# Kernel optimization log

Hardware: AMD Instinct MI355X
Metric: run time of the kernel (lower is better)

## Reference

```python
import jax, jax.numpy as jnp
import numpy as np

N = 50000      # nodes
E = 800000     # edges (before self-loops)
B = 512        # graphs in batch
IN, HID, OUT, HEADS = 768, 256, 128, 4
NEG_SLOPE = 0.2
EPS = 1e-16


def glorot(key, shape):
    fan = shape[0] + shape[-1]
    return jax.random.normal(key, shape, jnp.float32) * jnp.sqrt(2.0 / fan)


def setup_inputs() -> dict:
    key = jax.random.key(0)
    ks = jax.random.split(key, 12)
    d1, d2 = HID // HEADS, OUT // HEADS
    return {
        "x": jax.random.normal(ks[0], (N, IN), jnp.float32),
        "edge_index": jax.random.randint(ks[1], (2, E), 0, N),
        "batch": jnp.sort(jax.random.randint(ks[2], (N,), 0, B)),
        # conv1: GATConv(IN, HID//HEADS, heads=HEADS)
        "W1": glorot(ks[3], (IN, HID)),
        "att_src1": glorot(ks[4], (HEADS, d1)),
        "att_dst1": glorot(ks[5], (HEADS, d1)),
        "b1": jnp.zeros((HID,), jnp.float32),
        # conv2: GATConv(HID+IN, OUT//HEADS, heads=HEADS)
        "W2": glorot(ks[6], (HID + IN, OUT)),
        "att_src2": glorot(ks[7], (HEADS, d2)),
        "att_dst2": glorot(ks[8], (HEADS, d2)),
        "b2": jnp.zeros((OUT,), jnp.float32),
    }


def gat_conv(x, src, dst, W, att_src, att_dst, bias):
    # PyG GATConv (concat heads): h = x @ W, e_ij = LeakyReLU(a_s.h_j + a_d.h_i),
    # alpha = softmax over incoming edges of each destination node.
    n = x.shape[0]
    heads, d = att_src.shape
    h = (x @ W).reshape(n, heads, d)                          # [N,H,D]
    a_s = jnp.einsum('nhd,hd->nh', h, att_src)                # [N,H]
    a_d = jnp.einsum('nhd,hd->nh', h, att_dst)
    e = jax.nn.leaky_relu(a_s[src] + a_d[dst], NEG_SLOPE)     # [Etot,H]
    e_max = jax.ops.segment_max(e, dst, num_segments=n)
    e = jnp.exp(e - e_max[dst])
    denom = jax.ops.segment_sum(e, dst, num_segments=n)
    alpha = e / (denom[dst] + EPS)                            # [Etot,H]
    msg = h[src] * alpha[:, :, None]                          # [Etot,H,D]
    out = jax.ops.segment_sum(msg, dst, num_segments=n)       # [N,H,D]
    return out.reshape(n, heads * d) + bias


def reference(x, edge_index, batch, W1, att_src1, att_dst1, b1,
              W2, att_src2, att_dst2, b2):
    # BUrumorGAT swaps edge direction: row<->col
    src = edge_index[1]
    dst = edge_index[0]
    # PyG GATConv adds self-loops by default
    loops = jnp.arange(N)
    src = jnp.concatenate([src, loops])
    dst = jnp.concatenate([dst, loops])

    x1 = x  # original features
    h1 = gat_conv(x, src, dst, W1, att_src1, att_dst1, b1)    # [N,HID]
    x2 = h1

    # root of each graph = first node (in order) with that batch id
    roots = jax.ops.segment_min(jnp.arange(N), batch, num_segments=B)  # [B]
    re1 = x1[roots[batch]]                                    # [N,IN]
    xc = jax.nn.relu(jnp.concatenate([h1, re1], axis=1))      # [N,HID+IN]
    # F.dropout with training=False is identity (eval mode)

    h2 = jax.nn.relu(gat_conv(xc, src, dst, W2, att_src2, att_dst2, b2))  # [N,OUT]
    re2 = x2[roots[batch]]                                    # [N,HID]
    feat = jnp.concatenate([h2, re2], axis=1)                 # [N,OUT+HID]

    counts = jax.ops.segment_sum(jnp.ones((N,), jnp.float32), batch, num_segments=B)
    pooled = jax.ops.segment_sum(feat, batch, num_segments=B)
    return pooled / jnp.clip(counts, 1.0)[:, None]            # [B,OUT+HID]
```

## Files before the change

kernel.cpp:

```cpp
#include <hip/hip_runtime.h>

#define NN 50000
#define NBGRAPH 512
#define DIN 768
#define DHID 256
#define DOUT 128

typedef unsigned short ushort_t;
typedef __attribute__((ext_vector_type(4))) float f32x4;
typedef _Float16 f16_t;
typedef __attribute__((ext_vector_type(8))) _Float16 f16x8;

__device__ __forceinline__ float lrelu(float v) { return v > 0.f ? v : 0.2f * v; }

__device__ __forceinline__ float h2f_u(ushort_t u) { return (float)__builtin_bit_cast(f16_t, u); }
__device__ __forceinline__ ushort_t f2h_u(float f) { return __builtin_bit_cast(ushort_t, (f16_t)f); }

__device__ __forceinline__ float sel_h(int h, float q0, float q1, float q2, float q3) {
  float lo = (h & 1) ? q1 : q0;
  float hi = (h & 1) ? q3 : q2;
  return (h & 2) ? hi : lo;
}

__device__ __forceinline__ f16x8 cvt8(float4 u, float4 v) {
  unsigned int a = __builtin_bit_cast(unsigned int, __builtin_amdgcn_cvt_pkrtz(u.x, u.y));
  unsigned int b = __builtin_bit_cast(unsigned int, __builtin_amdgcn_cvt_pkrtz(u.z, u.w));
  unsigned int c = __builtin_bit_cast(unsigned int, __builtin_amdgcn_cvt_pkrtz(v.x, v.y));
  unsigned int d = __builtin_bit_cast(unsigned int, __builtin_amdgcn_cvt_pkrtz(v.z, v.w));
  uint4 q = {a, b, c, d};
  return __builtin_bit_cast(f16x8, q);
}
__device__ __forceinline__ f16x8 cvt8_relu(float4 u, float4 v) {
  u.x = fmaxf(u.x, 0.f); u.y = fmaxf(u.y, 0.f); u.z = fmaxf(u.z, 0.f); u.w = fmaxf(u.w, 0.f);
  v.x = fmaxf(v.x, 0.f); v.y = fmaxf(v.y, 0.f); v.z = fmaxf(v.z, 0.f); v.w = fmaxf(v.w, 0.f);
  return cvt8(u, v);
}

__global__ void k_zero2(int* __restrict__ a, int* __restrict__ b, int n) {
  int i = blockIdx.x * blockDim.x + threadIdx.x;
  if (i < n) { a[i] = 0; b[i] = 0; }
}

__global__ void k_hist(const int* __restrict__ ei, int* __restrict__ deg, int E, int Etot) {
  int e = blockIdx.x * blockDim.x + threadIdx.x;
  if (e >= Etot) return;
  int dst = (e < E) ? ei[e] : (e - E);
  atomicAdd(&deg[dst], 1);
}

__global__ __launch_bounds__(1024) void k_scan1(const int* __restrict__ deg, int* __restrict__ off,
                                                int* __restrict__ bsum, int n) {
  __shared__ int wsum[16];
  int tid = threadIdx.x, lane = tid & 63, w = tid >> 6;
  int i = blockIdx.x * 1024 + tid;
  int v = (i < n) ? deg[i] : 0;
  int x = v;
#pragma unroll
  for (int d = 1; d < 64; d <<= 1) { int t = __shfl_up(x, d); if (lane >= d) x += t; }
  if (lane == 63) wsum[w] = x;
  __syncthreads();
  if (tid < 16) {
    int y = wsum[tid];
#pragma unroll
    for (int d = 1; d < 16; d <<= 1) { int t = __shfl_up(y, d); if (tid >= d) y += t; }
    wsum[tid] = y;
  }
  __syncthreads();
  int base = (w > 0) ? wsum[w - 1] : 0;
  if (i < n) off[i] = base + x - v;
  if (tid == 1023) bsum[blockIdx.x] = wsum[15];
}

__global__ void k_scan2(int* __restrict__ bsum, int* __restrict__ off, int nb, int n) {
  int lane = threadIdx.x;
  int v = (lane < nb) ? bsum[lane] : 0;
  int x = v;
#pragma unroll
  for (int d = 1; d < 64; d <<= 1) { int t = __shfl_up(x, d); if (lane >= d) x += t; }
  if (lane < nb) bsum[lane] = x - v;
  if (lane == 63) off[n] = x;
}

__global__ void k_scan3(int* __restrict__ off, const int* __restrict__ bsum, int n) {
  int i = blockIdx.x * blockDim.x + threadIdx.x;
  if (i < n) off[i] += bsum[i >> 10];
}

__global__ void k_scatter(const int* __restrict__ ei, const int* __restrict__ off,
                          int* __restrict__ cur, int* __restrict__ csr, int E, int Etot) {
  int e = blockIdx.x * blockDim.x + threadIdx.x;
  if (e >= Etot) return;
  int dst, src;
  if (e < E) { dst = ei[e]; src = ei[E + e]; }
  else       { dst = src = e - E; }
  int p = atomicAdd(&cur[dst], 1);
  csr[off[dst] + p] = src;
}

__global__ void k_segstart(const int* __restrict__ batch, int* __restrict__ segstart, int n, int b_cnt) {
  int b = blockIdx.x * blockDim.x + threadIdx.x;
  if (b > b_cnt) return;
  int lo = 0, hi = n;
  while (lo < hi) { int mid = (lo + hi) >> 1; if (batch[mid] < b) lo = mid + 1; else hi = mid; }
  segstart[b] = lo;
}

__global__ void k_rootn(const int* __restrict__ batch, const int* __restrict__ segstart,
                        int* __restrict__ rootn, int n) {
  int i = blockIdx.x * blockDim.x + threadIdx.x;
  if (i < n) rootn[i] = segstart[batch[i]];
}

__global__ void k_prepW(const float* __restrict__ W, ushort_t* __restrict__ Wt, int K, int N) {
  int id = blockIdx.x * blockDim.x + threadIdx.x;
  if (id >= K * N) return;
  int n = id / K, k = id - n * K;
  Wt[(size_t)n * K + k] = f2h_u(W[(size_t)k * N + n]);
}

#define LDT2 72
__global__ __launch_bounds__(256) void k_gemm1m(const float* __restrict__ A,
                                                const ushort_t* __restrict__ Bt,
                                                ushort_t* __restrict__ C) {
  const int K = DIN, NC = DHID;
  __shared__ __align__(16) ushort_t As[64 * LDT2];
  __shared__ __align__(16) ushort_t Bs[128 * LDT2];
  const int tid = threadIdx.x;
  const int bm = blockIdx.x * 64;
  const int bn = blockIdx.y * 128;
  const int row = tid >> 2, q = tid & 3;
  const int arow = bm + row;
  const int r_c = arow < NN ? arow : NN - 1;
  const int wid = tid >> 6, lane = tid & 63;
  const int wr = (wid >> 1) * 32, wc = (wid & 1) * 64;
  const int fr = lane & 15, fg = lane >> 4;
  const float* aptr = &A[(size_t)r_c * K + q * 16];
  const int bc0 = tid >> 3, bk0 = tid & 7;
  const int bc1 = (tid + 256) >> 3, bk1 = (tid + 256) & 7;
  const int bc2 = (tid + 512) >> 3, bk2 = (tid + 512) & 7;
  const int bc3 = (tid + 768) >> 3, bk3 = (tid + 768) & 7;
  const ushort_t* bp0 = &Bt[(size_t)(bn + bc0) * K + bk0 * 8];
  const ushort_t* bp1 = &Bt[(size_t)(bn + bc1) * K + bk1 * 8];
  const ushort_t* bp2 = &Bt[(size_t)(bn + bc2) * K + bk2 * 8];
  const ushort_t* bp3 = &Bt[(size_t)(bn + bc3) * K + bk3 * 8];
  f32x4 acc[2][4] = {};

  float4 pa0, pa1, pa2, pa3;
  uint4 pb0, pb1, pb2, pb3;
  {
    const float4* s = (const float4*)aptr;
    pa0 = s[0]; pa1 = s[1]; pa2 = s[2]; pa3 = s[3];
    pb0 = *(const uint4*)bp0; pb1 = *(const uint4*)bp1;
    pb2 = *(const uint4*)bp2; pb3 = *(const uint4*)bp3;
  }

  for (int k0 = 0; k0 < K; k0 += 64) {
    {
      const int p = row * LDT2 + q * 16;
      f16x8 w0 = cvt8(pa0, pa1);
      f16x8 w1 = cvt8(pa2, pa3);
      *(f16x8*)&As[p + 0] = w0;
      *(f16x8*)&As[p + 8] = w1;
      *(uint4*)&Bs[bc0 * LDT2 + bk0 * 8] = pb0;
      *(uint4*)&Bs[bc1 * LDT2 + bk1 * 8] = pb1;
      *(uint4*)&Bs[bc2 * LDT2 + bk2 * 8] = pb2;
      *(uint4*)&Bs[bc3 * LDT2 + bk3 * 8] = pb3;
    }
    __syncthreads();
    const bool more = (k0 + 64) < K;
    float4 na0, na1, na2, na3;
    uint4 nb0, nb1, nb2, nb3;
    if (more) {
      const float4* s = (const float4*)(aptr + k0 + 64);
      na0 = s[0]; na1 = s[1]; na2 = s[2]; na3 = s[3];
      nb0 = *(const uint4*)(bp0 + k0 + 64); nb1 = *(const uint4*)(bp1 + k0 + 64);
      nb2 = *(const uint4*)(bp2 + k0 + 64); nb3 = *(const uint4*)(bp3 + k0 + 64);
    }
#pragma unroll
    for (int kk = 0; kk < 64; kk += 32) {
      f16x8 af0 = *(const f16x8*)&As[(wr + fr) * LDT2 + kk + fg * 8];
      f16x8 af1 = *(const f16x8*)&As[(wr + 16 + fr) * LDT2 + kk + fg * 8];
      f16x8 bf0 = *(const f16x8*)&Bs[(wc + fr) * LDT2 + kk + fg * 8];
      f16x8 bf1 = *(const f16x8*)&Bs[(wc + 16 + fr) * LDT2 + kk + fg * 8];
      f16x8 bf2 = *(const f16x8*)&Bs[(wc + 32 + fr) * LDT2 + kk + fg * 8];
      f16x8 bf3 = *(const f16x8*)&Bs[(wc + 48 + fr) * LDT2 + kk + fg * 8];
      acc[0][0] = __builtin_amdgcn_mfma_f32_16x16x32_f16(af0, bf0, acc[0][0], 0, 0, 0);
      acc[0][1] = __builtin_amdgcn_mfma_f32_16x16x32_f16(af0, bf1, acc[0][1], 0, 0, 0);
      acc[0][2] = __builtin_amdgcn_mfma_f32_16x16x32_f16(af0, bf2, acc[0][2], 0, 0, 0);
      acc[0][3] = __builtin_amdgcn_mfma_f32_16x16x32_f16(af0, bf3, acc[0][3], 0, 0, 0);
      acc[1][0] = __builtin_amdgcn_mfma_f32_16x16x32_f16(af1, bf0, acc[1][0], 0, 0, 0);
      acc[1][1] = __builtin_amdgcn_mfma_f32_16x16x32_f16(af1, bf1, acc[1][1], 0, 0, 0);
      acc[1][2] = __builtin_amdgcn_mfma_f32_16x16x32_f16(af1, bf2, acc[1][2], 0, 0, 0);
      acc[1][3] = __builtin_amdgcn_mfma_f32_16x16x32_f16(af1, bf3, acc[1][3], 0, 0, 0);
    }
    __syncthreads();
    if (more) {
      pa0 = na0; pa1 = na1; pa2 = na2; pa3 = na3;
      pb0 = nb0; pb1 = nb1; pb2 = nb2; pb3 = nb3;
    }
  }
#pragma unroll
  for (int m = 0; m < 2; ++m)
#pragma unroll
    for (int n = 0; n < 4; ++n)
#pragma unroll
      for (int j = 0; j < 4; ++j) {
        int r = bm + wr + m * 16 + fg * 4 + j;
        if (r < NN) C[(size_t)r * NC + bn + wc + n * 16 + fr] = f2h_u(acc[m][n][j]);
      }
}

__global__ __launch_bounds__(256) void k_gemm2m(const float* __restrict__ OUT1,
                                                const float* __restrict__ X,
                                                const int* __restrict__ rootn,
                                                const ushort_t* __restrict__ Bt,
                                                ushort_t* __restrict__ C) {
  const int K = DHID + DIN, NC = DOUT;
  __shared__ __align__(16) ushort_t As[64 * LDT2];
  __shared__ __align__(16) ushort_t Bs[128 * LDT2];
  const int tid = threadIdx.x;
  const int bm = blockIdx.x * 64;
  const int row = tid >> 2, q = tid & 3;
  const int arow = bm + row;
  const int r_c = arow < NN ? arow : NN - 1;
  const int rn = rootn[r_c];
  const int wid = tid >> 6, lane = tid & 63;
  const int wr = (wid >> 1) * 32, wc = (wid & 1) * 64;
  const int fr = lane & 15, fg = lane >> 4;
  const float* o1ptr = &OUT1[(size_t)r_c * DHID + q * 16];
  const float* xptr = &X[(size_t)rn * DIN + q * 16];
  const int bc0 = tid >> 3, bk0 = tid & 7;
  const int bc1 = (tid + 256) >> 3, bk1 = (tid + 256) & 7;
  const int bc2 = (tid + 512) >> 3, bk2 = (tid + 512) & 7;
  const int bc3 = (tid + 768) >> 3, bk3 = (tid + 768) & 7;
  const ushort_t* bp0 = &Bt[(size_t)bc0 * K + bk0 * 8];
  const ushort_t* bp1 = &Bt[(size_t)bc1 * K + bk1 * 8];
  const ushort_t* bp2 = &Bt[(size_t)bc2 * K + bk2 * 8];
  const ushort_t* bp3 = &Bt[(size_t)bc3 * K + bk3 * 8];
  f32x4 acc[2][4] = {};

  float4 pa0, pa1, pa2, pa3;
  uint4 pb0, pb1, pb2, pb3;
  {
    const float4* s = (const float4*)o1ptr;
    pa0 = s[0]; pa1 = s[1]; pa2 = s[2]; pa3 = s[3];
    pb0 = *(const uint4*)bp0; pb1 = *(const uint4*)bp1;
    pb2 = *(const uint4*)bp2; pb3 = *(const uint4*)bp3;
  }

  for (int k0 = 0; k0 < K; k0 += 64) {
    {
      const int p = row * LDT2 + q * 16;
      f16x8 w0 = cvt8_relu(pa0, pa1);
      f16x8 w1 = cvt8_relu(pa2, pa3);
      *(f16x8*)&As[p + 0] = w0;
      *(f16x8*)&As[p + 8] = w1;
      *(uint4*)&Bs[bc0 * LDT2 + bk0 * 8] = pb0;
      *(uint4*)&Bs[bc1 * LDT2 + bk1 * 8] = pb1;
      *(uint4*)&Bs[bc2 * LDT2 + bk2 * 8] = pb2;
      *(uint4*)&Bs[bc3 * LDT2 + bk3 * 8] = pb3;
    }
    __syncthreads();
    const bool more = (k0 + 64) < K;
    float4 na0, na1, na2, na3;
    uint4 nb0, nb1, nb2, nb3;
    if (more) {
      const int k0n = k0 + 64;
      const float4* s = (k0n < DHID) ? (const float4*)(o1ptr + k0n)
                                     : (const float4*)(xptr + (k0n - DHID));
      na0 = s[0]; na1 = s[1]; na2 = s[2]; na3 = s[3];
      nb0 = *(const uint4*)(bp0 + k0n); nb1 = *(const uint4*)(bp1 + k0n);
      nb2 = *(const uint4*)(bp2 + k0n); nb3 = *(const uint4*)(bp3 + k0n);
    }
#pragma unroll
    for (int kk = 0; kk < 64; kk += 32) {
      f16x8 af0 = *(const f16x8*)&As[(wr + fr) * LDT2 + kk + fg * 8];
      f16x8 af1 = *(const f16x8*)&As[(wr + 16 + fr) * LDT2 + kk + fg * 8];
      f16x8 bf0 = *(const f16x8*)&Bs[(wc + fr) * LDT2 + kk + fg * 8];
      f16x8 bf1 = *(const f16x8*)&Bs[(wc + 16 + fr) * LDT2 + kk + fg * 8];
      f16x8 bf2 = *(const f16x8*)&Bs[(wc + 32 + fr) * LDT2 + kk + fg * 8];
      f16x8 bf3 = *(const f16x8*)&Bs[(wc + 48 + fr) * LDT2 + kk + fg * 8];
      acc[0][0] = __builtin_amdgcn_mfma_f32_16x16x32_f16(af0, bf0, acc[0][0], 0, 0, 0);
      acc[0][1] = __builtin_amdgcn_mfma_f32_16x16x32_f16(af0, bf1, acc[0][1], 0, 0, 0);
      acc[0][2] = __builtin_amdgcn_mfma_f32_16x16x32_f16(af0, bf2, acc[0][2], 0, 0, 0);
      acc[0][3] = __builtin_amdgcn_mfma_f32_16x16x32_f16(af0, bf3, acc[0][3], 0, 0, 0);
      acc[1][0] = __builtin_amdgcn_mfma_f32_16x16x32_f16(af1, bf0, acc[1][0], 0, 0, 0);
      acc[1][1] = __builtin_amdgcn_mfma_f32_16x16x32_f16(af1, bf1, acc[1][1], 0, 0, 0);
      acc[1][2] = __builtin_amdgcn_mfma_f32_16x16x32_f16(af1, bf2, acc[1][2], 0, 0, 0);
      acc[1][3] = __builtin_amdgcn_mfma_f32_16x16x32_f16(af1, bf3, acc[1][3], 0, 0, 0);
    }
    __syncthreads();
    if (more) {
      pa0 = na0; pa1 = na1; pa2 = na2; pa3 = na3;
      pb0 = nb0; pb1 = nb1; pb2 = nb2; pb3 = nb3;
    }
  }
#pragma unroll
  for (int m = 0; m < 2; ++m)
#pragma unroll
    for (int n = 0; n < 4; ++n)
#pragma unroll
      for (int j = 0; j < 4; ++j) {
        int r = bm + wr + m * 16 + fg * 4 + j;
        if (r < NN) C[(size_t)r * NC + wc + n * 16 + fr] = f2h_u(acc[m][n][j]);
      }
}

__global__ __launch_bounds__(256) void k_scores1(const ushort_t* __restrict__ Hh,
                                                 const float* __restrict__ att_s,
                                                 const float* __restrict__ att_d,
                                                 float4* __restrict__ as_out,
                                                 float4* __restrict__ ad_out) {
  int lane = threadIdx.x & 63;
  int n = blockIdx.x * 4 + (threadIdx.x >> 6);
  if (n >= NN) return;
  ushort4 hv = *(const ushort4*)&Hh[(size_t)n * DHID + lane * 4];
  float h0 = h2f_u(hv.x), h1 = h2f_u(hv.y), h2 = h2f_u(hv.z), h3 = h2f_u(hv.w);
  float4 sa = *(const float4*)&att_s[lane * 4];
  float4 da = *(const float4*)&att_d[lane * 4];
  float ps = h0 * sa.x + h1 * sa.y + h2 * sa.z + h3 * sa.w;
  float pd = h0 * da.x + h1 * da.y + h2 * da.z + h3 * da.w;
#pragma unroll
  for (int m = 1; m < 16; m <<= 1) { ps += __shfl_xor(ps, m); pd += __shfl_xor(pd, m); }
  float4 rs, rd;
  rs.x = __shfl(ps, 0);  rd.x = __shfl(pd, 0);
  rs.y = __shfl(ps, 16); rd.y = __shfl(pd, 16);
  rs.z = __shfl(ps, 32); rd.z = __shfl(pd, 32);
  rs.w = __shfl(ps, 48); rd.w = __shfl(pd, 48);
  if (lane == 0) { as_out[n] = rs; ad_out[n] = rd; }
}

__global__ __launch_bounds__(256) void k_scores2(const ushort_t* __restrict__ Hh,
                                                 const float* __restrict__ att_s,
                                                 const float* __restrict__ att_d,
                                                 float4* __restrict__ as_out,
                                                 float4* __restrict__ ad_out) {
  int lane = threadIdx.x & 63;
  int n = blockIdx.x * 4 + (threadIdx.x >> 6);
  if (n >= NN) return;
  ushort2 hv = *(const ushort2*)&Hh[(size_t)n * DOUT + lane * 2];
  float h0 = h2f_u(hv.x), h1 = h2f_u(hv.y);
  float2 sa = *(const float2*)&att_s[lane * 2];
  float2 da = *(const float2*)&att_d[lane * 2];
  float ps = h0 * sa.x + h1 * sa.y;
  float pd = h0 * da.x + h1 * da.y;
#pragma unroll
  for (int m = 1; m < 16; m <<= 1) { ps += __shfl_xor(ps, m); pd += __shfl_xor(pd, m); }
  float4 rs, rd;
  rs.x = __shfl(ps, 0);  rd.x = __shfl(pd, 0);
  rs.y = __shfl(ps, 16); rd.y = __shfl(pd, 16);
  rs.z = __shfl(ps, 32); rd.z = __shfl(pd, 32);
  rs.w = __shfl(ps, 48); rd.w = __shfl(pd, 48);
  if (lane == 0) { as_out[n] = rs; ad_out[n] = rd; }
}

__global__ __launch_bounds__(256) void k_agg1(const int* __restrict__ off, const int* __restrict__ csr,
                                              const float4* __restrict__ as_v, const float4* __restrict__ ad_v,
                                              const ushort_t* __restrict__ Hh, const float* __restrict__ bias,
                                              float* __restrict__ OUT) {
  __shared__ int s_tab[16][65];
  __shared__ __align__(16) float al_tab[16][260];
  const int tid = threadIdx.x;
  const int nd = tid >> 4;
  const int g = tid & 15;
  const int hd = g >> 2;
  const int n = blockIdx.x * 16 + nd;
  if (n >= NN) return;
  const int beg = off[n];
  const int nt = off[n + 1] - beg;
  const float4 adv = ad_v[n];

  float acc[16] = {};
  float rdh;

  if (nt <= 64) {
    float mx0 = -INFINITY, mx1 = -INFINITY, mx2 = -INFINITY, mx3 = -INFINITY;
    for (int le = g; le < nt; le += 16) {
      int s = csr[beg + le];
      float4 a = as_v[s];
      s_tab[nd][le] = s;
      *(float4*)&al_tab[nd][le << 2] = a;
      mx0 = fmaxf(mx0, a.x); mx1 = fmaxf(mx1, a.y);
      mx2 = fmaxf(mx2, a.z); mx3 = fmaxf(mx3, a.w);
    }
#pragma unroll
    for (int m = 1; m < 16; m <<= 1) {
      mx0 = fmaxf(mx0, __shfl_xor(mx0, m)); mx1 = fmaxf(mx1, __shfl_xor(mx1, m));
      mx2 = fmaxf(mx2, __shfl_xor(mx2, m)); mx3 = fmaxf(mx3, __shfl_xor(mx3, m));
    }
    float em0 = lrelu(mx0 + adv.x), em1 = lrelu(mx1 + adv.y);
    float em2 = lrelu(mx2 + adv.z), em3 = lrelu(mx3 + adv.w);
    float s0 = 0.f, s1 = 0.f, s2 = 0.f, s3 = 0.f;
    for (int le = g; le < nt; le += 16) {
      float4 a = *(const float4*)&al_tab[nd][le << 2];
      float p0 = __expf(lrelu(a.x + adv.x) - em0);
      float p1 = __expf(lrelu(a.y + adv.y) - em1);
      float p2 = __expf(lrelu(a.z + adv.z) - em2);
      float p3 = __expf(lrelu(a.w + adv.w) - em3);
      *(float4*)&al_tab[nd][le << 2] = make_float4(p0, p1, p2, p3);
      s0 += p0; s1 += p1; s2 += p2; s3 += p3;
    }
#pragma unroll
    for (int m = 1; m < 16; m <<= 1) {
      s0 += __shfl_xor(s0, m); s1 += __shfl_xor(s1, m);
      s2 += __shfl_xor(s2, m); s3 += __shfl_xor(s3, m);
    }
    rdh = sel_h(hd, 1.f / (s0 + 1e-16f), 1.f / (s1 + 1e-16f),
                    1.f / (s2 + 1e-16f), 1.f / (s3 + 1e-16f));

    int sP = s_tab[nd][0];
    float pP = al_tab[nd][hd];
    f16x8 v0 = *(const f16x8*)&Hh[(size_t)sP * DHID + g * 16];
    f16x8 v1 = *(const f16x8*)&Hh[(size_t)sP * DHID + g * 16 + 8];
    for (int e = 0; e < nt; ++e) {
      int en = (e + 1 < nt) ? e + 1 : e;
      int sN = s_tab[nd][en];
      float pN = al_tab[nd][(en << 2) | hd];
      f16x8 n0 = *(const f16x8*)&Hh[(size_t)sN * DHID + g * 16];
      f16x8 n1 = *(const f16x8*)&Hh[(size_t)sN * DHID + g * 16 + 8];
      float al = pP * rdh;
#pragma unroll
      for (int q = 0; q < 8; ++q) acc[q] += al * (float)v0[q];
#pragma unroll
      for (int q = 0; q < 8; ++q) acc[8 + q] += al * (float)v1[q];
      pP = pN; v0 = n0; v1 = n1;
    }
  } else {
    float mx0 = -INFINITY, mx1 = -INFINITY, mx2 = -INFINITY, mx3 = -INFINITY;
    for (int le = g; le < nt; le += 16) {
      float4 a = as_v[csr[beg + le]];
      mx0 = fmaxf(mx0, a.x); mx1 = fmaxf(mx1, a.y);
      mx2 = fmaxf(mx2, a.z); mx3 = fmaxf(mx3, a.w);
    }
#pragma unroll
    for (int m = 1; m < 16; m <<= 1) {
      mx0 = fmaxf(mx0, __shfl_xor(mx0, m)); mx1 = fmaxf(mx1, __shfl_xor(mx1, m));
      mx2 = fmaxf(mx2, __shfl_xor(mx2, m)); mx3 = fmaxf(mx3, __shfl_xor(mx3, m));
    }
    float em0 = lrelu(mx0 + adv.x), em1 = lrelu(mx1 + adv.y);
    float em2 = lrelu(mx2 + adv.z), em3 = lrelu(mx3 + adv.w);
    float s0 = 0.f, s1 = 0.f, s2 = 0.f, s3 = 0.f;
    for (int le = g; le < nt; le += 16) {
      float4 a = as_v[csr[beg + le]];
      s0 += __expf(lrelu(a.x + adv.x) - em0);
      s1 += __expf(lrelu(a.y + adv.y) - em1);
      s2 += __expf(lrelu(a.z + adv.z) - em2);
      s3 += __expf(lrelu(a.w + adv.w) - em3);
    }
#pragma unroll
    for (int m = 1; m < 16; m <<= 1) {
      s0 += __shfl_xor(s0, m); s1 += __shfl_xor(s1, m);
      s2 += __shfl_xor(s2, m); s3 += __shfl_xor(s3, m);
    }
    rdh = sel_h(hd, 1.f / (s0 + 1e-16f), 1.f / (s1 + 1e-16f),
                    1.f / (s2 + 1e-16f), 1.f / (s3 + 1e-16f));
    float adh = sel_h(hd, adv.x, adv.y, adv.z, adv.w);
    float emh = sel_h(hd, em0, em1, em2, em3);
    for (int e = 0; e < nt; ++e) {
      int s = csr[beg + e];
      float4 a = as_v[s];
      float ah = sel_h(hd, a.x, a.y, a.z, a.w);
      float al = __expf(lrelu(ah + adh) - emh) * rdh;
      f16x8 v0 = *(const f16x8*)&Hh[(size_t)s * DHID + g * 16];
      f16x8 v1 = *(const f16x8*)&Hh[(size_t)s * DHID + g * 16 + 8];
#pragma unroll
      for (int q = 0; q < 8; ++q) acc[q] += al * (float)v0[q];
#pragma unroll
      for (int q = 0; q < 8; ++q) acc[8 + q] += al * (float)v1[q];
    }
  }

  const float* bv = &bias[g * 16];
  float* ob = &OUT[(size_t)n * DHID + g * 16];
#pragma unroll
  for (int k = 0; k < 4; ++k) {
    float4 b4 = *(const float4*)&bv[k * 4];
    *(float4*)&ob[k * 4] = make_float4(acc[k * 4] + b4.x, acc[k * 4 + 1] + b4.y,
                                       acc[k * 4 + 2] + b4.z, acc[k * 4 + 3] + b4.w);
  }
}

__global__ __launch_bounds__(256) void k_agg2(const int* __restrict__ off, const int* __restrict__ csr,
                                              const float4* __restrict__ as_v, const float4* __restrict__ ad_v,
                                              const ushort_t* __restrict__ Hh, const float* __restrict__ bias,
                                              float* __restrict__ OUT) {
  __shared__ int s_tab[16][65];
  __shared__ __align__(16) float al_tab[16][260];
  const int tid = threadIdx.x;
  const int nd = tid >> 4;
  const int g = tid & 15;
  const int hd = g >> 2;
  const int n = blockIdx.x * 16 + nd;
  if (n >= NN) return;
  const int beg = off[n];
  const int nt = off[n + 1] - beg;
  const float4 adv = ad_v[n];

  float acc[8] = {};
  float rdh;

  if (nt <= 64) {
    float mx0 = -INFINITY, mx1 = -INFINITY, mx2 = -INFINITY, mx3 = -INFINITY;
    for (int le = g; le < nt; le += 16) {
      int s = csr[beg + le];
      float4 a = as_v[s];
      s_tab[nd][le] = s;
      *(float4*)&al_tab[nd][le << 2] = a;
      mx0 = fmaxf(mx0, a.x); mx1 = fmaxf(mx1, a.y);
      mx2 = fmaxf(mx2, a.z); mx3 = fmaxf(mx3, a.w);
    }
#pragma unroll
    for (int m = 1; m < 16; m <<= 1) {
      mx0 = fmaxf(mx0, __shfl_xor(mx0, m)); mx1 = fmaxf(mx1, __shfl_xor(mx1, m));
      mx2 = fmaxf(mx2, __shfl_xor(mx2, m)); mx3 = fmaxf(mx3, __shfl_xor(mx3, m));
    }
    float em0 = lrelu(mx0 + adv.x), em1 = lrelu(mx1 + adv.y);
    float em2 = lrelu(mx2 + adv.z), em3 = lrelu(mx3 + adv.w);
    float s0 = 0.f, s1 = 0.f, s2 = 0.f, s3 = 0.f;
    for (int le = g; le < nt; le += 16) {
      float4 a = *(const float4*)&al_tab[nd][le << 2];
      float p0 = __expf(lrelu(a.x + adv.x) - em0);
      float p1 = __expf(lrelu(a.y + adv.y) - em1);
      float p2 = __expf(lrelu(a.z + adv.z) - em2);
      float p3 = __expf(lrelu(a.w + adv.w) - em3);
      *(float4*)&al_tab[nd][le << 2] = make_float4(p0, p1, p2, p3);
      s0 += p0; s1 += p1; s2 += p2; s3 += p3;
    }
#pragma unroll
    for (int m = 1; m < 16; m <<= 1) {
      s0 += __shfl_xor(s0, m); s1 += __shfl_xor(s1, m);
      s2 += __shfl_xor(s2, m); s3 += __shfl_xor(s3, m);
    }
    rdh = sel_h(hd, 1.f / (s0 + 1e-16f), 1.f / (s1 + 1e-16f),
                    1.f / (s2 + 1e-16f), 1.f / (s3 + 1e-16f));

    int sP = s_tab[nd][0];
    float pP = al_tab[nd][hd];
    f16x8 v0 = *(const f16x8*)&Hh[(size_t)sP * DOUT + g * 8];
    for (int e = 0; e < nt; ++e) {
      int en = (e + 1 < nt) ? e + 1 : e;
      int sN = s_tab[nd][en];
      float pN = al_tab[nd][(en << 2) | hd];
      f16x8 n0 = *(const f16x8*)&Hh[(size_t)sN * DOUT + g * 8];
      float al = pP * rdh;
#pragma unroll
      for (int q = 0; q < 8; ++q) acc[q] += al * (float)v0[q];
      pP = pN; v0 = n0;
    }
  } else {
    float mx0 = -INFINITY, mx1 = -INFINITY, mx2 = -INFINITY, mx3 = -INFINITY;
    for (int le = g; le < nt; le += 16) {
      float4 a = as_v[csr[beg + le]];
      mx0 = fmaxf(mx0, a.x); mx1 = fmaxf(mx1, a.y);
      mx2 = fmaxf(mx2, a.z); mx3 = fmaxf(mx3, a.w);
    }
#pragma unroll
    for (int m = 1; m < 16; m <<= 1) {
      mx0 = fmaxf(mx0, __shfl_xor(mx0, m)); mx1 = fmaxf(mx1, __shfl_xor(mx1, m));
      mx2 = fmaxf(mx2, __shfl_xor(mx2, m)); mx3 = fmaxf(mx3, __shfl_xor(mx3, m));
    }
    float em0 = lrelu(mx0 + adv.x), em1 = lrelu(mx1 + adv.y);
    float em2 = lrelu(mx2 + adv.z), em3 = lrelu(mx3 + adv.w);
    float s0 = 0.f, s1 = 0.f, s2 = 0.f, s3 = 0.f;
    for (int le = g; le < nt; le += 16) {
      float4 a = as_v[csr[beg + le]];
      s0 += __expf(lrelu(a.x + adv.x) - em0);
      s1 += __expf(lrelu(a.y + adv.y) - em1);
      s2 += __expf(lrelu(a.z + adv.z) - em2);
      s3 += __expf(lrelu(a.w + adv.w) - em3);
    }
#pragma unroll
    for (int m = 1; m < 16; m <<= 1) {
      s0 += __shfl_xor(s0, m); s1 += __shfl_xor(s1, m);
      s2 += __shfl_xor(s2, m); s3 += __shfl_xor(s3, m);
    }
    rdh = sel_h(hd, 1.f / (s0 + 1e-16f), 1.f / (s1 + 1e-16f),
                    1.f / (s2 + 1e-16f), 1.f / (s3 + 1e-16f));
    float adh = sel_h(hd, adv.x, adv.y, adv.z, adv.w);
    float emh = sel_h(hd, em0, em1, em2, em3);
    for (int e = 0; e < nt; ++e) {
      int s = csr[beg + e];
      float4 a = as_v[s];
      float ah = sel_h(hd, a.x, a.y, a.z, a.w);
      float al = __expf(lrelu(ah + adh) - emh) * rdh;
      f16x8 v0 = *(const f16x8*)&Hh[(size_t)s * DOUT + g * 8];
#pragma unroll
      for (int q = 0; q < 8; ++q) acc[q] += al * (float)v0[q];
    }
  }

  const float* bv = &bias[g * 8];
  float* ob = &OUT[(size_t)n * DOUT + g * 8];
#pragma unroll
  for (int k = 0; k < 2; ++k) {
    float4 b4 = *(const float4*)&bv[k * 4];
    *(float4*)&ob[k * 4] = make_float4(acc[k * 4] + b4.x, acc[k * 4 + 1] + b4.y,
                                       acc[k * 4 + 2] + b4.z, acc[k * 4 + 3] + b4.w);
  }
}

__global__ __launch_bounds__(256) void k_pool(const int* __restrict__ segstart,
                                              const float* __restrict__ OUT2,
                                              const float* __restrict__ OUT1,
                                              float* __restrict__ out) {
  int b = blockIdx.x;
  int t = threadIdx.x;
  int s = segstart[b], e = segstart[b + 1];
  float* ob = out + (size_t)b * 384;
  if (s >= e) {
    for (int i = t; i < 384; i += 256) ob[i] = 0.f;
    return;
  }
  if (t < 128) {
    float s0 = 0.f, s1 = 0.f;
    int n = s;
    for (; n + 1 < e; n += 2) {
      float v0 = OUT2[(size_t)n * DOUT + t];
      float v1 = OUT2[(size_t)(n + 1) * DOUT + t];
      s0 += fmaxf(v0, 0.f); s1 += fmaxf(v1, 0.f);
    }
    if (n < e) s0 += fmaxf(OUT2[(size_t)n * DOUT + t], 0.f);
    ob[t] = (s0 + s1) / (float)(e - s);
  } else {
    int k = t - 128;
    ob[128 + k] = OUT1[(size_t)s * DHID + k];
    ob[256 + k] = OUT1[(size_t)s * DHID + 128 + k];
  }
}

extern "C" void kernel_launch(void* const* d_in, const int* in_sizes, int n_in,
                              void* d_out, int out_size, void* d_ws, size_t ws_size,
                              hipStream_t stream) {
  const float* x    = (const float*)d_in[0];
  const int*   ei   = (const int*)d_in[1];
  const int*   batch = (const int*)d_in[2];
  const float* W1   = (const float*)d_in[3];
  const float* as1w = (const float*)d_in[4];
  const float* ad1w = (const float*)d_in[5];
  const float* b1   = (const float*)d_in[6];
  const float* W2   = (const float*)d_in[7];
  const float* as2w = (const float*)d_in[8];
  const float* ad2w = (const float*)d_in[9];
  const float* b2   = (const float*)d_in[10];
  float* out = (float*)d_out;
  char* ws = (char*)d_ws;

  const int E = in_sizes[1] / 2;
  const int Etot = E + NN;

  ushort_t* H1h = (ushort_t*)(ws + 0);
  ushort_t* H2h = (ushort_t*)(ws + 0);
  ushort_t* Wt2h = (ushort_t*)(ws + 13000000);
  float*  OUT2 = (float*)(ws + 25600000);
  float*  OUT1 = (float*)(ws + 51200000);
  float4* as1  = (float4*)(ws + 102400000);
  float4* ad1  = (float4*)(ws + 103200000);
  float4* as2  = (float4*)(ws + 104000000);
  float4* ad2  = (float4*)(ws + 104800000);
  int* deg     = (int*)(ws + 105600000);
  int* cur     = (int*)(ws + 105800000);
  int* off     = (int*)(ws + 106000000);
  int* csr     = (int*)(ws + 106200016);
  int* segstart = (int*)(ws + 109600016);
  int* rootn   = (int*)(ws + 109602080);
  int* bsum    = (int*)(ws + 109802080);
  ushort_t* Wt1h = (ushort_t*)(ws + 105600000);

  const int TB = 256;
  const int NB_SCAN = (NN + 1023) / 1024;

  k_zero2<<<(NN + TB - 1) / TB, TB, 0, stream>>>(deg, cur, NN);
  k_hist<<<(Etot + TB - 1) / TB, TB, 0, stream>>>(ei, deg, E, Etot);
  k_scan1<<<NB_SCAN, 1024, 0, stream>>>(deg, off, bsum, NN);
  k_scan2<<<1, 64, 0, stream>>>(bsum, off, NB_SCAN, NN);
  k_scan3<<<NB_SCAN, 1024, 0, stream>>>(off, bsum, NN);
  k_scatter<<<(Etot + TB - 1) / TB, TB, 0, stream>>>(ei, off, cur, csr, E, Etot);
  k_segstart<<<(NBGRAPH + 1 + TB - 1) / TB, TB, 0, stream>>>(batch, segstart, NN, NBGRAPH);
  k_rootn<<<(NN + TB - 1) / TB, TB, 0, stream>>>(batch, segstart, rootn, NN);

  k_prepW<<<(DIN * DHID + TB - 1) / TB, TB, 0, stream>>>(W1, Wt1h, DIN, DHID);
  dim3 g1((NN + 63) / 64, DHID / 128);
  k_gemm1m<<<g1, TB, 0, stream>>>(x, Wt1h, H1h);
  k_scores1<<<(NN + 3) / 4, TB, 0, stream>>>(H1h, as1w, ad1w, as1, ad1);
  k_agg1<<<(NN + 15) / 16, TB, 0, stream>>>(off, csr, as1, ad1, H1h, b1, OUT1);

  k_prepW<<<((DHID + DIN) * DOUT + TB - 1) / TB, TB, 0, stream>>>(W2, Wt2h, DHID + DIN, DOUT);
  dim3 g2((NN + 63) / 64, 1);
  k_gemm2m<<<g2, TB, 0, stream>>>(OUT1, x, rootn, Wt2h, H2h);
  k_scores2<<<(NN + 3) / 4, TB, 0, stream>>>(H2h, as2w, ad2w, as2, ad2);
  k_agg2<<<(NN + 15) / 16, TB, 0, stream>>>(off, csr, as2, ad2, H2h, b2, OUT2);

  k_pool<<<NBGRAPH, TB, 0, stream>>>(segstart, OUT2, OUT1, out);
}
```

Measured before the change: 349.2 us.

## Precompute per-graph root-feature projection and shrink second GEMM K dimension

After: 344.2 us. About the same (-1.4%).

```diff
diff --git a/kernel.cpp b/kernel.cpp
--- a/kernel.cpp
+++ b/kernel.cpp
@@ -210,12 +210,40 @@
       }
 }
 
+__global__ __launch_bounds__(256) void k_gemmR(const float* __restrict__ X,
+                                               const int* __restrict__ segstart,
+                                               const ushort_t* __restrict__ Wt2,
+                                               float* __restrict__ R2) {
+  __shared__ float part[2][128];
+  const int b = blockIdx.x;
+  const int t = threadIdx.x;
+  const int c = t & 127, seg = t >> 7;
+  int root = segstart[b];
+  if (root >= NN) root = NN - 1;
+  const float* xr = &X[(size_t)root * DIN + seg * 384];
+  const ushort_t* wp = &Wt2[(size_t)c * (DHID + DIN) + DHID + seg * 384];
+  float s = 0.f;
+#pragma unroll 4
+  for (int k = 0; k < 384; k += 4) {
+    float4 xv = *(const float4*)&xr[k];
+    ushort4 wv = *(const ushort4*)&wp[k];
+    s += fmaxf(xv.x, 0.f) * h2f_u(wv.x);
+    s += fmaxf(xv.y, 0.f) * h2f_u(wv.y);
+    s += fmaxf(xv.z, 0.f) * h2f_u(wv.z);
+    s += fmaxf(xv.w, 0.f) * h2f_u(wv.w);
+  }
+  part[seg][c] = s;
+  __syncthreads();
+  if (t < 128) R2[(size_t)b * DOUT + t] = part[0][t] + part[1][t];
+}
+
 __global__ __launch_bounds__(256) void k_gemm2m(const float* __restrict__ OUT1,
-                                                const float* __restrict__ X,
-                                                const int* __restrict__ rootn,
+                                                const int* __restrict__ batch,
                                                 const ushort_t* __restrict__ Bt,
+                                                const float* __restrict__ R2,
                                                 ushort_t* __restrict__ C) {
-  const int K = DHID + DIN, NC = DOUT;
+  const int K = DHID;
+  const int KS = DHID + DIN;
   __shared__ __align__(16) ushort_t As[64 * LDT2];
   __shared__ __align__(16) ushort_t Bs[128 * LDT2];
   const int tid = threadIdx.x;
@@ -223,26 +251,24 @@
   const int row = tid >> 2, q = tid & 3;
   const int arow = bm + row;
   const int r_c = arow < NN ? arow : NN - 1;
-  const int rn = rootn[r_c];
   const int wid = tid >> 6, lane = tid & 63;
   const int wr = (wid >> 1) * 32, wc = (wid & 1) * 64;
   const int fr = lane & 15, fg = lane >> 4;
-  const float* o1ptr = &OUT1[(size_t)r_c * DHID + q * 16];
-  const float* xptr = &X[(size_t)rn * DIN + q * 16];
+  const float* aptr = &OUT1[(size_t)r_c * DHID + q * 16];
   const int bc0 = tid >> 3, bk0 = tid & 7;
   const int bc1 = (tid + 256) >> 3, bk1 = (tid + 256) & 7;
   const int bc2 = (tid + 512) >> 3, bk2 = (tid + 512) & 7;
   const int bc3 = (tid + 768) >> 3, bk3 = (tid + 768) & 7;
-  const ushort_t* bp0 = &Bt[(size_t)bc0 * K + bk0 * 8];
-  const ushort_t* bp1 = &Bt[(size_t)bc1 * K + bk1 * 8];
-  const ushort_t* bp2 = &Bt[(size_t)bc2 * K + bk2 * 8];
-  const ushort_t* bp3 = &Bt[(size_t)bc3 * K + bk3 * 8];
+  const ushort_t* bp0 = &Bt[(size_t)bc0 * KS + bk0 * 8];
+  const ushort_t* bp1 = &Bt[(size_t)bc1 * KS + bk1 * 8];
+  const ushort_t* bp2 = &Bt[(size_t)bc2 * KS + bk2 * 8];
+  const ushort_t* bp3 = &Bt[(size_t)bc3 * KS + bk3 * 8];
   f32x4 acc[2][4] = {};
 
   float4 pa0, pa1, pa2, pa3;
   uint4 pb0, pb1, pb2, pb3;
   {
-    const float4* s = (const float4*)o1ptr;
+    const float4* s = (const float4*)aptr;
     pa0 = s[0]; pa1 = s[1]; pa2 = s[2]; pa3 = s[3];
     pb0 = *(const uint4*)bp0; pb1 = *(const uint4*)bp1;
     pb2 = *(const uint4*)bp2; pb3 = *(const uint4*)bp3;
@@ -265,12 +291,10 @@
     float4 na0, na1, na2, na3;
     uint4 nb0, nb1, nb2, nb3;
     if (more) {
-      const int k0n = k0 + 64;
-      const float4* s = (k0n < DHID) ? (const float4*)(o1ptr + k0n)
-                                     : (const float4*)(xptr + (k0n - DHID));
+      const float4* s = (const float4*)(aptr + k0 + 64);
       na0 = s[0]; na1 = s[1]; na2 = s[2]; na3 = s[3];
-      nb0 = *(const uint4*)(bp0 + k0n); nb1 = *(const uint4*)(bp1 + k0n);
-      nb2 = *(const uint4*)(bp2 + k0n); nb3 = *(const uint4*)(bp3 + k0n);
+      nb0 = *(const uint4*)(bp0 + k0 + 64); nb1 = *(const uint4*)(bp1 + k0 + 64);
+      nb2 = *(const uint4*)(bp2 + k0 + 64); nb3 = *(const uint4*)(bp3 + k0 + 64);
     }
 #pragma unroll
     for (int kk = 0; kk < 64; kk += 32) {
@@ -298,12 +322,18 @@
 #pragma unroll
   for (int m = 0; m < 2; ++m)
 #pragma unroll
-    for (int n = 0; n < 4; ++n)
-#pragma unroll
-      for (int j = 0; j < 4; ++j) {
-        int r = bm + wr + m * 16 + fg * 4 + j;
-        if (r < NN) C[(size_t)r * NC + wc + n * 16 + fr] = f2h_u(acc[m][n][j]);
+    for (int j = 0; j < 4; ++j) {
+      int r = bm + wr + m * 16 + fg * 4 + j;
+      if (r < NN) {
+        int gb = batch[r];
+        const float* r2 = &R2[(size_t)gb * DOUT];
+#pragma unroll
+        for (int n = 0; n < 4; ++n) {
+          int col = wc + n * 16 + fr;
+          C[(size_t)r * DOUT + col] = f2h_u(acc[m][n][j] + r2[col]);
+        }
       }
+    }
 }
 
 __global__ __launch_bounds__(256) void k_scores1(const ushort_t* __restrict__ Hh,
@@ -651,6 +681,7 @@
   ushort_t* H1h = (ushort_t*)(ws + 0);
   ushort_t* H2h = (ushort_t*)(ws + 0);
   ushort_t* Wt2h = (ushort_t*)(ws + 13000000);
+  float*  R2   = (float*)(ws + 14000000);
   float*  OUT2 = (float*)(ws + 25600000);
   float*  OUT1 = (float*)(ws + 51200000);
   float4* as1  = (float4*)(ws + 102400000);
@@ -685,8 +716,9 @@
   k_agg1<<<(NN + 15) / 16, TB, 0, stream>>>(off, csr, as1, ad1, H1h, b1, OUT1);
 
   k_prepW<<<((DHID + DIN) * DOUT + TB - 1) / TB, TB, 0, stream>>>(W2, Wt2h, DHID + DIN, DOUT);
+  k_gemmR<<<NBGRAPH, TB, 0, stream>>>(x, segstart, Wt2h, R2);
   dim3 g2((NN + 63) / 64, 1);
-  k_gemm2m<<<g2, TB, 0, stream>>>(OUT1, x, rootn, Wt2h, H2h);
+  k_gemm2m<<<g2, TB, 0, stream>>>(OUT1, batch, Wt2h, R2, H2h);
   k_scores2<<<(NN + 3) / 4, TB, 0, stream>>>(H2h, as2w, ad2w, as2, ad2);
   k_agg2<<<(NN + 15) / 16, TB, 0, stream>>>(off, csr, as2, ad2, H2h, b2, OUT2);
 
```
